# Kernel tuning notes

Hardware: AMD Instinct MI355X
Metric: run time of the kernel (lower is better)

Reference implementation:

```python
import jax, jax.numpy as jnp
import numpy as np

B, L, D = 8, 2048, 256


def setup_inputs() -> dict:
    key = jax.random.key(0)
    k1, k2, k3, k4, k5, k6 = jax.random.split(key, 6)
    c1 = jax.random.normal(k1, (B, L, D), dtype=jnp.float32)
    c2 = jax.random.normal(k2, (B, L, D), dtype=jnp.float32)
    c_mask = jnp.zeros((B, L), dtype=bool)  # True = padded position
    # FusionLayer params: linear_f: (4D -> D), linear_g: (4D -> 1)
    s = 1.0 / np.sqrt(4 * D)
    W_f = jax.random.uniform(k3, (4 * D, D), dtype=jnp.float32, minval=-s, maxval=s)
    b_f = jax.random.uniform(k4, (D,), dtype=jnp.float32, minval=-s, maxval=s)
    W_g = jax.random.uniform(k5, (4 * D, 1), dtype=jnp.float32, minval=-s, maxval=s)
    b_g = jax.random.uniform(k6, (1,), dtype=jnp.float32, minval=-s, maxval=s)
    return {"c1": c1, "c2": c2, "c_mask": c_mask, "W_f": W_f, "b_f": b_f,
            "W_g": W_g, "b_g": b_g, "flag": 1}


def reference(c1, c2, c_mask, W_f, b_f, W_g, b_g, flag):
    # flag == 1 -> forward_fuse path
    # AttentionScore default (correlation_func=1): scores[b,i,j] = c2[b,i] . c1[b,j]
    scores = jnp.einsum('bid,bjd->bij', c2, c1)  # [B, L, L]
    neg_inf = jnp.array(-jnp.inf, dtype=scores.dtype)
    diag = jnp.eye(scores.shape[1], dtype=bool)[None]        # [1, L, L]
    scores = jnp.where(diag, neg_inf, scores)                 # mask self-attention diag
    scores = jnp.where(c_mask[:, None, :], neg_inf, scores)   # mask padded keys
    alpha = jax.nn.softmax(scores, axis=2)                    # [B, L, L]
    aug_c2 = jnp.einsum('bij,bjd->bid', alpha, c1)            # [B, L, D]
    # FusionLayer: z = [x, y, x*y, x-y]; out = g*tanh(Wf z) + (1-g)*x
    z = jnp.concatenate([c2, aug_c2, c2 * aug_c2, c2 - aug_c2], axis=2)  # [B, L, 4D]
    gated = jax.nn.sigmoid(z @ W_g + b_g)                     # [B, L, 1]
    fusion = jnp.tanh(z @ W_f + b_f)                          # [B, L, D]
    return gated * fusion + (1.0 - gated) * c2
```

## Files before the change

### kernel.cpp

```cpp
#include <hip/hip_runtime.h>
#include <math.h>

#define BB 8
#define LL 2048
#define DD 256

typedef float  f4_t __attribute__((ext_vector_type(4)));
typedef short  s8_t __attribute__((ext_vector_type(8)));

union S8U { s8_t v; unsigned u[4]; };

__device__ __forceinline__ unsigned bitsf(float x){ union{float f; unsigned u;} c; c.f=x; return c.u; }
__device__ __forceinline__ float fbits(unsigned u){ union{float f; unsigned u;} c; c.u=u; return c.f; }
__device__ __forceinline__ unsigned pkhi(float a, float b){ return (bitsf(a)>>16) | (bitsf(b)&0xffff0000u); }
__device__ __forceinline__ unsigned pkrn(float a, float b){
    unsigned ua = bitsf(a) + 0x8000u, ub = bitsf(b) + 0x8000u;
    return (ua>>16) | (ub&0xffff0000u);
}
__device__ __forceinline__ short rnb(float a){ return (short)((bitsf(a) + 0x8000u) >> 16); }

__device__ __forceinline__ int vslot(int e){ return ((e>>2)&3)*8 + ((e>>4)<<2) + (e&3); }

__global__ __launch_bounds__(512,1)
void attn_kernel(const float* __restrict__ c1, const float* __restrict__ c2,
                 const unsigned char* __restrict__ cmask,
                 float* __restrict__ o0, float* __restrict__ o1,
                 float* __restrict__ mlp,
                 int klen, int split)
{
    __shared__ short    KhiS[2][32*264];
    __shared__ unsigned VpS [2][256*20];

    const int tid  = threadIdx.x;
    const int lane = tid & 63;
    const int w    = tid >> 6;
    const int il   = lane & 15;
    const int quad = lane >> 4;
    const int col  = tid & 255;
    const int hr   = (tid >> 8) * 16;

    const int blk  = blockIdx.x;
    const int bb   = blk & 7;
    const int qb   = (blk >> 3) & 15;
    const int half = split ? ((blk >> 7) & 1) : 0;
    const int kb   = half * klen;

    float* ob = half ? o1 : o0;

    const float* c1b = c1 + (size_t)bb * LL * DD;
    const float* c2b = c2 + (size_t)bb * LL * DD;
    const unsigned char* mb = cmask + (size_t)bb * LL;

    const int q0w = qb*128 + w*16;

    s8_t qh[8], ql[8];
    {
        const float* qp = c2b + (size_t)(q0w + il)*DD + quad*8;
#pragma unroll
        for (int kd = 0; kd < 8; ++kd) {
            float4 x0 = *(const float4*)(qp + kd*32);
            float4 x1 = *(const float4*)(qp + kd*32 + 4);
            float e[8] = {x0.x,x0.y,x0.z,x0.w,x1.x,x1.y,x1.z,x1.w};
            S8U h, l;
#pragma unroll
            for (int p2 = 0; p2 < 4; ++p2) {
                float a = e[2*p2], b = e[2*p2+1];
                h.u[p2] = pkhi(a, b);
                float alo = a - fbits(bitsf(a)&0xffff0000u);
                float blo = b - fbits(bitsf(b)&0xffff0000u);
                l.u[p2] = pkhi(alo, blo);
            }
            qh[kd] = h.v; ql[kd] = l.v;
        }
    }

    f4_t o[16];
#pragma unroll
    for (int n = 0; n < 16; ++n) o[n] = (f4_t)0.0f;
    float m_s = -INFINITY;
    float l_s = 0.f;

    const int NT = klen >> 5;
    float g[16];

#define STAGE_WRITE(KH, VP) do { \
    _Pragma("unroll") \
    for (int e_ = 0; e_ < 16; ++e_) \
        (KH)[(hr + e_)*264 + col] = rnb(g[e_]); \
    _Pragma("unroll") \
    for (int e_ = 0; e_ < 16; e_ += 2) \
        (VP)[col*20 + (vslot(hr + e_)>>1)] = pkrn(g[e_], g[e_+1]); \
} while (0)

#pragma unroll
    for (int e = 0; e < 16; ++e) g[e] = c1b[(size_t)(kb + hr + e)*DD + col];
    STAGE_WRITE(KhiS[0], VpS[0]);
    __syncthreads();

    int cur = 0;
    for (int kt = 0; kt < NT; ++kt) {
        const int k0 = kt << 5;
        if (kt + 1 < NT) {
#pragma unroll
            for (int e = 0; e < 16; ++e)
                g[e] = c1b[(size_t)(kb + k0 + 32 + hr + e)*DD + col];
        }

        const short*    Khi = KhiS[cur];
        const unsigned* Vp  = VpS[cur];

        f4_t acc[2];
        acc[0] = (f4_t)0.0f;
        acc[1] = (f4_t)0.0f;

#pragma unroll
        for (int kd = 0; kd < 8; ++kd) {
            s8_t ah0 = *(const s8_t*)&Khi[(il     )*264 + kd*32 + quad*8];
            s8_t ah1 = *(const s8_t*)&Khi[(16 + il)*264 + kd*32 + quad*8];
            acc[0] = __builtin_amdgcn_mfma_f32_16x16x32_bf16(ah0, qh[kd], acc[0], 0,0,0);
            acc[1] = __builtin_amdgcn_mfma_f32_16x16x32_bf16(ah1, qh[kd], acc[1], 0,0,0);
            acc[0] = __builtin_amdgcn_mfma_f32_16x16x32_bf16(ah0, ql[kd], acc[0], 0,0,0);
            acc[1] = __builtin_amdgcn_mfma_f32_16x16x32_bf16(ah1, ql[kd], acc[1], 0,0,0);
        }

        unsigned mu[2];
#pragma unroll
        for (int mj = 0; mj < 2; ++mj)
            mu[mj] = *(const unsigned*)(mb + kb + k0 + 16*mj + 4*quad);

        const int ig = q0w + il;
        float tm = -INFINITY;
        f4_t p[2];
#pragma unroll
        for (int mj = 0; mj < 2; ++mj) {
#pragma unroll
            for (int b = 0; b < 4; ++b) {
                int jg = kb + k0 + 16*mj + 4*quad + b;
                float s = acc[mj][b];
                bool dead = (((mu[mj] >> (8*b)) & 0xff) != 0) || (jg == ig);
                s = dead ? -INFINITY : s;
                p[mj][b] = s;
                tm = fmaxf(tm, s);
            }
        }
        tm = fmaxf(tm, __shfl_xor(tm, 16, 64));
        tm = fmaxf(tm, __shfl_xor(tm, 32, 64));
        const bool stable = __all(tm <= m_s);
        const float mn = stable ? m_s : fmaxf(m_s, tm);
        float rs = 0.f;
#pragma unroll
        for (int mj = 0; mj < 2; ++mj) {
#pragma unroll
            for (int b = 0; b < 4; ++b) {
                float pe = __expf(p[mj][b] - mn);
                p[mj][b] = pe;
                rs += pe;
            }
        }
        rs += __shfl_xor(rs, 16, 64);
        rs += __shfl_xor(rs, 32, 64);
        if (!stable) {
            float al = __expf(m_s - mn);
            l_s = l_s*al + rs;
            m_s = mn;
            float am[4];
#pragma unroll
            for (int b = 0; b < 4; ++b) am[b] = __shfl(al, 4*quad + b, 64);
#pragma unroll
            for (int n = 0; n < 16; ++n) {
#pragma unroll
                for (int b = 0; b < 4; ++b) o[n][b] *= am[b];
            }
        } else {
            l_s += rs;
        }

        s8_t ap;
        {
            S8U a;
            a.u[0] = pkrn(p[0][0], p[0][1]);
            a.u[1] = pkrn(p[0][2], p[0][3]);
            a.u[2] = pkrn(p[1][0], p[1][1]);
            a.u[3] = pkrn(p[1][2], p[1][3]);
            ap = a.v;
        }
#pragma unroll
        for (int n = 0; n < 16; ++n) {
            s8_t bv = *(const s8_t*)(Vp + (16*n + il)*20 + quad*4);
            o[n] = __builtin_amdgcn_mfma_f32_16x16x32_bf16(ap, bv, o[n], 0,0,0);
        }

        if (kt + 1 < NT) {
            short*    KhiN = KhiS[cur^1];
            unsigned* VpN  = VpS[cur^1];
            STAGE_WRITE(KhiN, VpN);
        }
        __syncthreads();
        cur ^= 1;
    }
#undef STAGE_WRITE

    const int rbq = bb*LL + q0w;
    if (split) {
        const int rbase = rbq + 4*quad;
#pragma unroll
        for (int n = 0; n < 16; ++n) {
            const int d = 16*n + il;
#pragma unroll
            for (int b = 0; b < 4; ++b)
                ob[(size_t)(rbase + b)*DD + d] = o[n][b];
        }
        if (lane < 16) {
            int r = rbq + lane;
            *(float2*)(&mlp[((size_t)half*16384 + r)*2]) = make_float2(m_s, l_s);
        }
    } else {
        float invl[4];
#pragma unroll
        for (int b = 0; b < 4; ++b) invl[b] = 1.0f / __shfl(l_s, 4*quad + b, 64);
        const int rbase = rbq + 4*quad;
#pragma unroll
        for (int n = 0; n < 16; ++n) {
            const int d = 16*n + il;
#pragma unroll
            for (int b = 0; b < 4; ++b)
                ob[(size_t)(rbase + b)*DD + d] = o[n][b] * invl[b];
        }
    }
}

__global__ __launch_bounds__(256)
void prep_kernel(const float* __restrict__ Wf, const float* __restrict__ Wg,
                 unsigned* __restrict__ Whi, unsigned* __restrict__ Wlo,
                 float* __restrict__ gw)
{
    if (blockIdx.x == 384) {
#pragma unroll
        for (int i = 0; i < 3; ++i) {
            int kl = threadIdx.x;
            float v = (i == 0) ? (Wg[kl] + Wg[768 + kl])
                    : (i == 1) ? (Wg[256 + kl] - Wg[768 + kl])
                               :  Wg[512 + kl];
            gw[i*256 + kl] = v;
        }
        return;
    }
    int t    = blockIdx.x*256 + threadIdx.x;
    int p    = t & 3;
    int lane = (t >> 2) & 63;
    int nt   = (t >> 8) & 15;
    int g2   = t >> 12;
    int seg  = g2 % 3;
    int kc   = g2 / 3;
    int kl   = kc*32 + (lane >> 4)*8 + 2*p;
    int n    = nt*16 + (lane & 15);
    float v0, v1;
    if (seg == 0) {
        v0 = Wf[(size_t)kl*DD + n]       + Wf[(size_t)(768 + kl)*DD + n];
        v1 = Wf[(size_t)(kl + 1)*DD + n] + Wf[(size_t)(769 + kl)*DD + n];
    } else if (seg == 1) {
        v0 = Wf[(size_t)(256 + kl)*DD + n] - Wf[(size_t)(768 + kl)*DD + n];
        v1 = Wf[(size_t)(257 + kl)*DD + n] - Wf[(size_t)(769 + kl)*DD + n];
    } else {
        v0 = Wf[(size_t)(512 + kl)*DD + n];
        v1 = Wf[(size_t)(513 + kl)*DD + n];
    }
    Whi[t] = pkhi(v0, v1);
    float l0 = v0 - fbits(bitsf(v0) & 0xffff0000u);
    float l1 = v1 - fbits(bitsf(v1) & 0xffff0000u);
    Wlo[t] = pkrn(l0, l1);
}

__global__ __launch_bounds__(512,1)
void fusion_mfma(const float* __restrict__ c2,
                 const float* __restrict__ P0, const float* __restrict__ P1,
                 const float* __restrict__ mlp,
                 const unsigned* __restrict__ Whi, const unsigned* __restrict__ Wlo,
                 const float* __restrict__ gw, const float* __restrict__ bg,
                 const float* __restrict__ bf, float* __restrict__ out, int ns)
{
    __shared__ float    gwL[768];
    __shared__ unsigned zA[2][64*20];
    __shared__ unsigned zB[2][64*20];
    __shared__ unsigned zC[2][64*20];
    __shared__ float    gpart[64][8];
    __shared__ float    gv[64];

    const int tid  = threadIdx.x;
    const int lane = tid & 63;
    const int w    = tid >> 6;
    const int il   = lane & 15;
    const int quad = lane >> 4;
    const int srow = tid >> 3;
    const int scg  = tid & 7;
    const size_t row0 = (size_t)blockIdx.x * 64;

    const float* c2b = c2 + row0*DD;
    const float* P0b = P0 + row0*DD;
    const float* P1b = P1 + row0*DD;

    for (int i = tid; i < 768; i += 512) gwL[i] = gw[i];

    float ca0 = 1.f, ca1 = 0.f;
    if (ns == 2) {
        const size_t r = row0 + srow;
        float m0 = mlp[r*2],             l0 = mlp[r*2 + 1];
        float m1 = mlp[(16384 + r)*2],   l1 = mlp[(16384 + r)*2 + 1];
        float M  = fmaxf(m0, m1);
        float a0 = __expf(m0 - M), a1 = __expf(m1 - M);
        float inv = 1.0f / (a0*l0 + a1*l1);
        ca0 = a0*inv; ca1 = a1*inv;
    }
    __syncthreads();

    float gatep = 0.f;
    float4 pr4; f4_t u4;

#define FLOAD(kc_) do { \
    const int off_ = srow*DD + (kc_)*32 + scg*4; \
    pr4 = *(const float4*)(c2b + off_); \
    u4  = *(const f4_t*)(P0b + off_); \
    if (ns == 2) { \
        f4_t v4_ = *(const f4_t*)(P1b + off_); \
        u4 = u4*ca0 + v4_*ca1; \
    } \
} while (0)

#define FCONV(buf_, kc_) do { \
    const int co_ = (kc_)*32 + scg*4; \
    float ea0_ = pr4.x, ea1_ = pr4.y, ea2_ = pr4.z, ea3_ = pr4.w; \
    float d0_ = ea0_*u4[0], d1_ = ea1_*u4[1], d2_ = ea2_*u4[2], d3_ = ea3_*u4[3]; \
    gatep += ea0_*gwL[co_+0] + u4[0]*gwL[256+co_+0] + d0_*gwL[512+co_+0] \
           + ea1_*gwL[co_+1] + u4[1]*gwL[256+co_+1] + d1_*gwL[512+co_+1] \
           + ea2_*gwL[co_+2] + u4[2]*gwL[256+co_+2] + d2_*gwL[512+co_+2] \
           + ea3_*gwL[co_+3] + u4[3]*gwL[256+co_+3] + d3_*gwL[512+co_+3]; \
    const int zi_ = srow*20 + scg*2; \
    *(uint2*)&zA[buf_][zi_] = make_uint2(pkrn(ea0_, ea1_), pkrn(ea2_, ea3_)); \
    *(uint2*)&zB[buf_][zi_] = make_uint2(pkrn(u4[0], u4[1]), pkrn(u4[2], u4[3])); \
    *(uint2*)&zC[buf_][zi_] = make_uint2(pkrn(d0_, d1_),   pkrn(d2_, d3_)); \
} while (0)

    f4_t acc[4][2];
#pragma unroll
    for (int mt = 0; mt < 4; ++mt)
#pragma unroll
        for (int nt = 0; nt < 2; ++nt) acc[mt][nt] = (f4_t)0.0f;

    FLOAD(0); FCONV(0, 0);
    __syncthreads();

    int cur = 0;
    for (int kc = 0; kc < 8; ++kc) {
        if (kc + 1 < 8) FLOAD(kc + 1);

        s8_t fa[4], fb[4], fc[4];
#pragma unroll
        for (int mt = 0; mt < 4; ++mt) {
            const int fi = (16*mt + il)*20 + quad*4;
            fa[mt] = *(const s8_t*)&zA[cur][fi];
            fb[mt] = *(const s8_t*)&zB[cur][fi];
            fc[mt] = *(const s8_t*)&zC[cur][fi];
        }
#pragma unroll
        for (int nt = 0; nt < 2; ++nt) {
            const int ntg = w*2 + nt;
            const size_t f0 = ((size_t)((kc*3 + 0)*16 + ntg)*64 + lane)*4;
            const size_t f1 = ((size_t)((kc*3 + 1)*16 + ntg)*64 + lane)*4;
            const size_t f2 = ((size_t)((kc*3 + 2)*16 + ntg)*64 + lane)*4;
            s8_t w0h = *(const s8_t*)(Whi + f0), w0l = *(const s8_t*)(Wlo + f0);
            s8_t w1h = *(const s8_t*)(Whi + f1), w1l = *(const s8_t*)(Wlo + f1);
            s8_t w2h = *(const s8_t*)(Whi + f2), w2l = *(const s8_t*)(Wlo + f2);
#pragma unroll
            for (int mt = 0; mt < 4; ++mt) {
                acc[mt][nt] = __builtin_amdgcn_mfma_f32_16x16x32_bf16(fa[mt], w0h, acc[mt][nt], 0,0,0);
                acc[mt][nt] = __builtin_amdgcn_mfma_f32_16x16x32_bf16(fa[mt], w0l, acc[mt][nt], 0,0,0);
                acc[mt][nt] = __builtin_amdgcn_mfma_f32_16x16x32_bf16(fb[mt], w1h, acc[mt][nt], 0,0,0);
                acc[mt][nt] = __builtin_amdgcn_mfma_f32_16x16x32_bf16(fb[mt], w1l, acc[mt][nt], 0,0,0);
                acc[mt][nt] = __builtin_amdgcn_mfma_f32_16x16x32_bf16(fc[mt], w2h, acc[mt][nt], 0,0,0);
                acc[mt][nt] = __builtin_amdgcn_mfma_f32_16x16x32_bf16(fc[mt], w2l, acc[mt][nt], 0,0,0);
            }
        }

        if (kc + 1 < 8) FCONV(cur ^ 1, kc + 1);
        __syncthreads();
        cur ^= 1;
    }
#undef FLOAD
#undef FCONV

    gpart[srow][scg] = gatep;
    __syncthreads();
    if (tid < 64) {
        float s = 0.f;
#pragma unroll
        for (int cg = 0; cg < 8; ++cg) s += gpart[tid][cg];
        gv[tid] = 1.0f / (1.0f + __expf(-(s + bg[0])));
    }
    __syncthreads();

#pragma unroll
    for (int nt = 0; nt < 2; ++nt) {
        const int col = w*32 + nt*16 + il;
        const float bfv = bf[col];
#pragma unroll
        for (int mt = 0; mt < 4; ++mt) {
#pragma unroll
            for (int b = 0; b < 4; ++b) {
                const int r = 16*mt + 4*quad + b;
                const float g = gv[r];
                const float cc = c2b[(size_t)r*DD + col];
                out[(row0 + r)*DD + col] = g * tanhf(acc[mt][nt][b] + bfv) + (1.f - g) * cc;
            }
        }
    }
}

extern "C" void kernel_launch(void* const* d_in, const int* in_sizes, int n_in,
                              void* d_out, int out_size, void* d_ws, size_t ws_size,
                              hipStream_t stream)
{
    const float* c1 = (const float*)d_in[0];
    const float* c2 = (const float*)d_in[1];
    const unsigned char* cmask = (const unsigned char*)d_in[2];
    const float* Wf = (const float*)d_in[3];
    const float* bf = (const float*)d_in[4];
    const float* Wg = (const float*)d_in[5];
    const float* bg = (const float*)d_in[6];

    const size_t aug_elems   = (size_t)16384 * 256;
    const size_t frag_elems  = (size_t)98304;

    const size_t ml2_elems = (size_t)2 * 16384 * 2;
    const size_t need2     = (2*aug_elems + ml2_elems + aug_elems) * sizeof(float);

    float* wsf = (float*)d_ws;

    if (ws_size >= need2) {
        float* Op0 = wsf;
        float* Op1 = wsf + aug_elems;
        float* mlp = wsf + 2*aug_elems;
        unsigned* Whi = (unsigned*)(wsf + 2*aug_elems + ml2_elems);
        unsigned* Wlo = Whi + frag_elems;
        float*    gw  = (float*)(Wlo + frag_elems);

        attn_kernel<<<dim3(256), dim3(512), 0, stream>>>(c1, c2, cmask,
                                                         Op0, Op1, mlp, 1024, 1);
        prep_kernel<<<dim3(385), dim3(256), 0, stream>>>(Wf, Wg, Whi, Wlo, gw);
        fusion_mfma<<<dim3(256), dim3(512), 0, stream>>>(c2, Op0, Op1, mlp,
                                                         Whi, Wlo, gw, bg, bf,
                                                         (float*)d_out, 2);
    } else {
        float* aug = wsf;
        unsigned* Whi = (unsigned*)(wsf + aug_elems);
        unsigned* Wlo = Whi + frag_elems;
        float*    gw  = (float*)(Wlo + frag_elems);

        attn_kernel<<<dim3(128), dim3(512), 0, stream>>>(c1, c2, cmask,
                                                         aug, aug, wsf, 2048, 0);
        prep_kernel<<<dim3(385), dim3(256), 0, stream>>>(Wf, Wg, Whi, Wlo, gw);
        fusion_mfma<<<dim3(256), dim3(512), 0, stream>>>(c2, aug, aug, wsf,
                                                         Whi, Wlo, gw, bg, bf,
                                                         (float*)d_out, 1);
    }
}
```

Before: 204.3 us.

## Fold weight prep into attention launch and XOR-swizzle V LDS layout

The separate weight-preparation kernel is merged into the attention kernel as extra trailing blocks (192 fragment blocks plus one gate-weight block), removing one launch and letting prep run on idle CUs alongside attention. The V tile in shared memory is XOR-swizzled on write and read to reduce LDS bank conflicts on the MFMA B-operand loads. Prep blocks still reserve the attention kernel's large static LDS and 512-thread shape, which may limit co-residency.

```diff
diff --git a/kernel.cpp b/kernel.cpp
--- a/kernel.cpp
+++ b/kernel.cpp
@@ -26,10 +26,55 @@
                  const unsigned char* __restrict__ cmask,
                  float* __restrict__ o0, float* __restrict__ o1,
                  float* __restrict__ mlp,
-                 int klen, int split)
+                 const float* __restrict__ Wf, const float* __restrict__ Wg,
+                 unsigned* __restrict__ Whi, unsigned* __restrict__ Wlo,
+                 float* __restrict__ gw,
+                 int klen, int split, int nattn)
 {
     __shared__ short    KhiS[2][32*264];
     __shared__ unsigned VpS [2][256*20];
+
+    if ((int)blockIdx.x >= nattn) {
+        const int pb  = blockIdx.x - nattn;
+        const int ptid = threadIdx.x;
+        if (pb == 192) {
+            if (ptid < 256) {
+#pragma unroll
+                for (int i = 0; i < 3; ++i) {
+                    float v = (i == 0) ? (Wg[ptid] + Wg[768 + ptid])
+                            : (i == 1) ? (Wg[256 + ptid] - Wg[768 + ptid])
+                                       :  Wg[512 + ptid];
+                    gw[i*256 + ptid] = v;
+                }
+            }
+            return;
+        }
+        int t    = pb*512 + ptid;
+        int p    = t & 3;
+        int lane = (t >> 2) & 63;
+        int nt   = (t >> 8) & 15;
+        int g2   = t >> 12;
+        int seg  = g2 % 3;
+        int kc   = g2 / 3;
+        int kl   = kc*32 + (lane >> 4)*8 + 2*p;
+        int n    = nt*16 + (lane & 15);
+        float v0, v1;
+        if (seg == 0) {
+            v0 = Wf[(size_t)kl*DD + n]       + Wf[(size_t)(768 + kl)*DD + n];
+            v1 = Wf[(size_t)(kl + 1)*DD + n] + Wf[(size_t)(769 + kl)*DD + n];
+        } else if (seg == 1) {
+            v0 = Wf[(size_t)(256 + kl)*DD + n] - Wf[(size_t)(768 + kl)*DD + n];
+            v1 = Wf[(size_t)(257 + kl)*DD + n] - Wf[(size_t)(769 + kl)*DD + n];
+        } else {
+            v0 = Wf[(size_t)(512 + kl)*DD + n];
+            v1 = Wf[(size_t)(513 + kl)*DD + n];
+        }
+        Whi[t] = pkhi(v0, v1);
+        float l0 = v0 - fbits(bitsf(v0) & 0xffff0000u);
+        float l1 = v1 - fbits(bitsf(v1) & 0xffff0000u);
+        Wlo[t] = pkrn(l0, l1);
+        return;
+    }
 
     const int tid  = threadIdx.x;
     const int lane = tid & 63;
@@ -38,6 +83,7 @@
     const int quad = lane >> 4;
     const int col  = tid & 255;
     const int hr   = (tid >> 8) * 16;
+    const int xv   = (col >> 3) & 3;
 
     const int blk  = blockIdx.x;
     const int bb   = blk & 7;
@@ -88,8 +134,10 @@
     for (int e_ = 0; e_ < 16; ++e_) \
         (KH)[(hr + e_)*264 + col] = rnb(g[e_]); \
     _Pragma("unroll") \
-    for (int e_ = 0; e_ < 16; e_ += 2) \
-        (VP)[col*20 + (vslot(hr + e_)>>1)] = pkrn(g[e_], g[e_+1]); \
+    for (int e_ = 0; e_ < 16; e_ += 2) { \
+        const int s_ = vslot(hr + e_) >> 1; \
+        (VP)[col*20 + (((s_ >> 2) ^ xv) << 2) + (s_ & 3)] = pkrn(g[e_], g[e_+1]); \
+    } \
 } while (0)
 
 #pragma unroll
@@ -186,7 +234,8 @@
         }
 #pragma unroll
         for (int n = 0; n < 16; ++n) {
-            s8_t bv = *(const s8_t*)(Vp + (16*n + il)*20 + quad*4);
+            const int vr = 16*n + il;
+            s8_t bv = *(const s8_t*)(Vp + vr*20 + ((quad ^ ((vr >> 3) & 3)) << 2));
             o[n] = __builtin_amdgcn_mfma_f32_16x16x32_bf16(ap, bv, o[n], 0,0,0);
         }
 
@@ -227,48 +276,6 @@
                 ob[(size_t)(rbase + b)*DD + d] = o[n][b] * invl[b];
         }
     }
-}
-
-__global__ __launch_bounds__(256)
-void prep_kernel(const float* __restrict__ Wf, const float* __restrict__ Wg,
-                 unsigned* __restrict__ Whi, unsigned* __restrict__ Wlo,
-                 float* __restrict__ gw)
-{
-    if (blockIdx.x == 384) {
-#pragma unroll
-        for (int i = 0; i < 3; ++i) {
-            int kl = threadIdx.x;
-            float v = (i == 0) ? (Wg[kl] + Wg[768 + kl])
-                    : (i == 1) ? (Wg[256 + kl] - Wg[768 + kl])
-                               :  Wg[512 + kl];
-            gw[i*256 + kl] = v;
-        }
-        return;
-    }
-    int t    = blockIdx.x*256 + threadIdx.x;
-    int p    = t & 3;
-    int lane = (t >> 2) & 63;
-    int nt   = (t >> 8) & 15;
-    int g2   = t >> 12;
-    int seg  = g2 % 3;
-    int kc   = g2 / 3;
-    int kl   = kc*32 + (lane >> 4)*8 + 2*p;
-    int n    = nt*16 + (lane & 15);
-    float v0, v1;
-    if (seg == 0) {
-        v0 = Wf[(size_t)kl*DD + n]       + Wf[(size_t)(768 + kl)*DD + n];
-        v1 = Wf[(size_t)(kl + 1)*DD + n] + Wf[(size_t)(769 + kl)*DD + n];
-    } else if (seg == 1) {
-        v0 = Wf[(size_t)(256 + kl)*DD + n] - Wf[(size_t)(768 + kl)*DD + n];
-        v1 = Wf[(size_t)(257 + kl)*DD + n] - Wf[(size_t)(769 + kl)*DD + n];
-    } else {
-        v0 = Wf[(size_t)(512 + kl)*DD + n];
-        v1 = Wf[(size_t)(513 + kl)*DD + n];
-    }
-    Whi[t] = pkhi(v0, v1);
-    float l0 = v0 - fbits(bitsf(v0) & 0xffff0000u);
-    float l1 = v1 - fbits(bitsf(v1) & 0xffff0000u);
-    Wlo[t] = pkrn(l0, l1);
 }
 
 __global__ __launch_bounds__(512,1)
@@ -443,9 +450,10 @@
         unsigned* Wlo = Whi + frag_elems;
         float*    gw  = (float*)(Wlo + frag_elems);
 
-        attn_kernel<<<dim3(256), dim3(512), 0, stream>>>(c1, c2, cmask,
-                                                         Op0, Op1, mlp, 1024, 1);
-        prep_kernel<<<dim3(385), dim3(256), 0, stream>>>(Wf, Wg, Whi, Wlo, gw);
+        attn_kernel<<<dim3(449), dim3(512), 0, stream>>>(c1, c2, cmask,
+                                                         Op0, Op1, mlp,
+                                                         Wf, Wg, Whi, Wlo, gw,
+                                                         1024, 1, 256);
         fusion_mfma<<<dim3(256), dim3(512), 0, stream>>>(c2, Op0, Op1, mlp,
                                                          Whi, Wlo, gw, bg, bf,
                                                          (float*)d_out, 2);
@@ -455,9 +463,10 @@
         unsigned* Wlo = Whi + frag_elems;
         float*    gw  = (float*)(Wlo + frag_elems);
 
-        attn_kernel<<<dim3(128), dim3(512), 0, stream>>>(c1, c2, cmask,
-                                                         aug, aug, wsf, 2048, 0);
-        prep_kernel<<<dim3(385), dim3(256), 0, stream>>>(Wf, Wg, Whi, Wlo, gw);
+        attn_kernel<<<dim3(321), dim3(512), 0, stream>>>(c1, c2, cmask,
+                                                         aug, aug, wsf,
+                                                         Wf, Wg, Whi, Wlo, gw,
+                                                         2048, 0, 128);
         fusion_mfma<<<dim3(256), dim3(512), 0, stream>>>(c2, aug, aug, wsf,
                                                          Whi, Wlo, gw, bg, bf,
                                                          (float*)d_out, 1);
```

Result: no change. 200.8 us (-1.7%).
